# Optimization experiments

Measured on AMD Instinct MI355X. Metric: run time of the kernel, lower is better.

The kernel has to match this reference:

```python
import jax, jax.numpy as jnp
import numpy as np

H = 16  # num_attention_heads
LN_EPS = 1e-12


def setup_inputs() -> dict:
    key = jax.random.key(0)
    ks = jax.random.split(key, 13)
    S, B, D = 2048, 2, 1024
    std = 0.02
    return {
        "query_tensor": jax.random.normal(ks[0], (S, B, D), jnp.float32),
        "key_tensor": jax.random.normal(ks[1], (S, B, D), jnp.float32),
        "value_tensor": jax.random.normal(ks[2], (S, B, D), jnp.float32),
        "Wq": jax.random.normal(ks[3], (D, D), jnp.float32) * std,
        "bq": jnp.zeros((D,), jnp.float32),
        "Wk": jax.random.normal(ks[4], (D, D), jnp.float32) * std,
        "bk": jnp.zeros((D,), jnp.float32),
        "Wv": jax.random.normal(ks[5], (D, D), jnp.float32) * std,
        "bv": jnp.zeros((D,), jnp.float32),
        "Wo": jax.random.normal(ks[6], (D, D), jnp.float32) * std,
        "bo": jnp.zeros((D,), jnp.float32),
        "ln_w": jnp.ones((D,), jnp.float32),
        "ln_b": jnp.zeros((D,), jnp.float32),
    }


def _layernorm(x, w, b):
    u = jnp.mean(x, axis=-1, keepdims=True)
    s = jnp.mean(jnp.square(x - u), axis=-1, keepdims=True)
    return w * ((x - u) / jnp.sqrt(s + LN_EPS)) + b


def reference(query_tensor, key_tensor, value_tensor, Wq, bq, Wk, bk, Wv, bv, Wo, bo, ln_w, ln_b):
    S, B, D = query_tensor.shape
    dh = D // H
    # QKV projections (nn.Linear: x @ W.T + b)
    q = query_tensor @ Wq.T + bq          # (S, B, D)
    k = key_tensor @ Wk.T + bk            # (Sk, B, D)
    v = value_tensor @ Wv.T + bv          # (Sk, B, D)
    # (S, B, D) -> (B*H, S, dh)
    q = q.reshape(S, B * H, dh).transpose(1, 0, 2)
    k = k.reshape(-1, B * H, dh).transpose(1, 0, 2)
    v = v.reshape(-1, B * H, dh).transpose(1, 0, 2)
    # NOTE: original code has NO 1/sqrt(dh) scaling
    scores = jnp.einsum('nqd,nkd->nqk', q, k)            # (B*H, S, Sk)
    probs = jax.nn.softmax(scores, axis=-1)
    # dropout is identity in eval mode
    ctx = jnp.einsum('nqk,nkd->nqd', probs, v)           # (B*H, S, dh)
    ctx = ctx.transpose(1, 0, 2).reshape(S, B, D)
    # BertSelfOutput: dense + residual + LayerNorm (dropout identity)
    out = ctx @ Wo.T + bo
    return _layernorm(out + query_tensor, ln_w, ln_b)
```

## Files before the change

### kernel.cpp

```cpp
#include <hip/hip_runtime.h>

#define SEQ    2048
#define BATCH  2
#define DMODEL 1024
#define NHEAD  16
#define DH     64
#define MROWS  (SEQ*BATCH)
#define RS     (BATCH*DMODEL)
#define LN_EPS 1e-12f

typedef __attribute__((ext_vector_type(8))) short short8;
typedef __attribute__((ext_vector_type(4))) float floatx4;

#define AS_GLOBAL __attribute__((address_space(1)))
#define AS_LDS    __attribute__((address_space(3)))

__device__ __forceinline__ float bf2f(unsigned short s) {
    union { unsigned u; float f; } a; a.u = ((unsigned)s) << 16; return a.f;
}
__device__ __forceinline__ unsigned short f2bf(float x) {
    union { float f; unsigned u; } a; a.f = x;
    unsigned r = a.u + 0x7fffu + ((a.u >> 16) & 1u);
    return (unsigned short)(r >> 16);
}
__device__ __forceinline__ unsigned cvt_pk_bf16(float a, float b) {
    unsigned r;
    asm("v_cvt_pk_bf16_f32 %0, %1, %2" : "=v"(r) : "v"(a), "v"(b));
    return r;
}
__device__ __forceinline__ uint4 cvt8(const float* __restrict__ p) {
    float4 x0 = *(const float4*)(p);
    float4 x1 = *(const float4*)(p + 4);
    union { uint4 u; unsigned short s[8]; } r;
    r.s[0] = f2bf(x0.x); r.s[1] = f2bf(x0.y);
    r.s[2] = f2bf(x0.z); r.s[3] = f2bf(x0.w);
    r.s[4] = f2bf(x1.x); r.s[5] = f2bf(x1.y);
    r.s[6] = f2bf(x1.z); r.s[7] = f2bf(x1.w);
    return r.u;
}

__global__ void beacon_kernel(float* out, float val) {
    if (threadIdx.x == 0) out[0] = val;
}

__global__ __launch_bounds__(256)
void cvt_kernel(const float* __restrict__ s0, const float* __restrict__ s1,
                const float* __restrict__ s2, const float* __restrict__ s3,
                const float* __restrict__ s4, const float* __restrict__ s5,
                const float* __restrict__ s6,
                unsigned short* __restrict__ d0, unsigned short* __restrict__ d1,
                unsigned short* __restrict__ d2, unsigned short* __restrict__ d3,
                unsigned short* __restrict__ d4, unsigned short* __restrict__ d5,
                unsigned short* __restrict__ d6)
{
    const float* srcs[7] = {s0, s1, s2, s3, s4, s5, s6};
    unsigned short* dsts[7] = {d0, d1, d2, d3, d4, d5, d6};
    const int cnts[7] = {4194304, 4194304, 4194304, 1048576, 1048576, 1048576, 1048576};
    const int z = blockIdx.z;
    const float* src = srcs[z];
    unsigned short* dst = dsts[z];
    const int count = cnts[z];
    const int stride = gridDim.x * 256 * 8;
    for (int i = (blockIdx.x * 256 + threadIdx.x) * 8; i < count; i += stride)
        *(uint4*)&dst[i] = cvt8(&src[i]);
}

__global__ __launch_bounds__(256)
void vt_kernel(const unsigned short* __restrict__ Vb,
               unsigned short* __restrict__ VT)
{
    __shared__ __align__(16) short T[64*72];
    const int tid = threadIdx.x;
    const int s0 = blockIdx.x * 64;
    const int bh = blockIdx.y;
    const int b = bh >> 4, h = bh & 15;

    #pragma unroll
    for (int rep = 0; rep < 2; ++rep) {
        int c = tid + rep * 256;
        int s = c >> 3, cc = c & 7;
        *(uint4*)&T[s*72 + cc*8] =
            *(const uint4*)&Vb[((s0 + s) * BATCH + b) * DMODEL + h*64 + cc*8];
    }
    __syncthreads();
    #pragma unroll
    for (int rep = 0; rep < 2; ++rep) {
        int o = tid + rep * 256;
        int d = o >> 3, sc = o & 7;
        union { uint4 u; unsigned short e[8]; } pk;
        #pragma unroll
        for (int j = 0; j < 8; ++j)
            pk.e[j] = (unsigned short)T[(sc*8 + j)*72 + d];
        *(uint4*)&VT[bh*(DH*SEQ) + d*SEQ + s0 + sc*8] = pk.u;
    }
}

template<int OUTF32>
__device__ __forceinline__ void gemm_bf16_body(
    const unsigned short* __restrict__ A,
    const unsigned short* __restrict__ W,
    const float* __restrict__ bias,
    void* __restrict__ Cout)
{
    __shared__ __align__(16) short Alds[128*32];
    __shared__ __align__(16) short Blds[128*32];

    const int tid  = threadIdx.x;
    const int lane = tid & 63;
    const int wave = tid >> 6;
    const int lrow = lane & 15;
    const int lq   = lane >> 4;
    const int m0 = blockIdx.x * 128;
    const int n0 = blockIdx.y * 128;
    const int mw = (wave >> 1) * 64;
    const int nw = (wave & 1) * 64;
    const int K  = DMODEL;

    const int chunk0 = tid;
    const int chunk1 = tid + 256;
    const int row0 = chunk0 >> 2, col0 = (chunk0 & 3) << 3;
    const int row1 = chunk1 >> 2, col1 = (chunk1 & 3) << 3;
    const unsigned short* gA0 = &A[(m0 + row0) * K + col0];
    const unsigned short* gA1 = &A[(m0 + row1) * K + col1];
    const unsigned short* gB0 = &W[(n0 + row0) * K + col0];
    const unsigned short* gB1 = &W[(n0 + row1) * K + col1];
    AS_LDS unsigned int* lA0 = (AS_LDS unsigned int*)&Alds[(wave*64)*8];
    AS_LDS unsigned int* lA1 = (AS_LDS unsigned int*)&Alds[(256 + wave*64)*8];
    AS_LDS unsigned int* lB0 = (AS_LDS unsigned int*)&Blds[(wave*64)*8];
    AS_LDS unsigned int* lB1 = (AS_LDS unsigned int*)&Blds[(256 + wave*64)*8];

    floatx4 zero = {0.f, 0.f, 0.f, 0.f};
    floatx4 acc[4][4];
    #pragma unroll
    for (int i = 0; i < 4; ++i)
        #pragma unroll
        for (int j = 0; j < 4; ++j) acc[i][j] = zero;

    for (int k0 = 0; k0 < K; k0 += 32) {
        __builtin_amdgcn_global_load_lds((const AS_GLOBAL unsigned int*)(gA0 + k0), lA0, 16, 0, 0);
        __builtin_amdgcn_global_load_lds((const AS_GLOBAL unsigned int*)(gA1 + k0), lA1, 16, 0, 0);
        __builtin_amdgcn_global_load_lds((const AS_GLOBAL unsigned int*)(gB0 + k0), lB0, 16, 0, 0);
        __builtin_amdgcn_global_load_lds((const AS_GLOBAL unsigned int*)(gB1 + k0), lB1, 16, 0, 0);
        __syncthreads();
        short8 af[4], bfg[4];
        #pragma unroll
        for (int mi = 0; mi < 4; ++mi)
            af[mi] = *(const short8*)&Alds[(mw + mi*16 + lrow)*32 + lq*8];
        #pragma unroll
        for (int ni = 0; ni < 4; ++ni)
            bfg[ni] = *(const short8*)&Blds[(nw + ni*16 + lrow)*32 + lq*8];
        #pragma unroll
        for (int mi = 0; mi < 4; ++mi)
            #pragma unroll
            for (int ni = 0; ni < 4; ++ni)
                acc[mi][ni] = __builtin_amdgcn_mfma_f32_16x16x32_bf16(af[mi], bfg[ni], acc[mi][ni], 0, 0, 0);
        __syncthreads();
    }

    #pragma unroll
    for (int mi = 0; mi < 4; ++mi) {
        #pragma unroll
        for (int ni = 0; ni < 4; ++ni) {
            int n = n0 + nw + ni*16 + lrow;
            float bv_ = bias[n];
            #pragma unroll
            for (int r = 0; r < 4; ++r) {
                int m = m0 + mw + mi*16 + lq*4 + r;
                float v = acc[mi][ni][r] + bv_;
                if (OUTF32) ((float*)Cout)[m * DMODEL + n] = v;
                else ((unsigned short*)Cout)[m * DMODEL + n] = f2bf(v);
            }
        }
    }
}

__global__ __launch_bounds__(256)
void qkv_bf16(const unsigned short* __restrict__ qb, const unsigned short* __restrict__ kb,
              const unsigned short* __restrict__ vb,
              const unsigned short* __restrict__ Wqb, const float* __restrict__ bq,
              const unsigned short* __restrict__ Wkb, const float* __restrict__ bk,
              const unsigned short* __restrict__ Wvb, const float* __restrict__ bv,
              unsigned short* __restrict__ Qo, unsigned short* __restrict__ Ko,
              unsigned short* __restrict__ Vo)
{
    const unsigned short *A, *W; const float* B; unsigned short* C;
    if (blockIdx.z == 0)      { A = qb; W = Wqb; B = bq; C = Qo; }
    else if (blockIdx.z == 1) { A = kb; W = Wkb; B = bk; C = Ko; }
    else                      { A = vb; W = Wvb; B = bv; C = Vo; }
    gemm_bf16_body<0>(A, W, B, C);
}

__global__ __launch_bounds__(256)
void oproj_bf16(const unsigned short* __restrict__ Cx,
                const unsigned short* __restrict__ Wob, const float* __restrict__ bo,
                float* __restrict__ O32)
{
    gemm_bf16_body<1>(Cx, Wob, bo, O32);
}

__global__ __launch_bounds__(256)
void qkv_mfma(const float* __restrict__ q_in, const float* __restrict__ k_in,
              const float* __restrict__ v_in,
              const float* __restrict__ Wq, const float* __restrict__ bq,
              const float* __restrict__ Wk, const float* __restrict__ bk,
              const float* __restrict__ Wv, const float* __restrict__ bv,
              unsigned short* __restrict__ Qo, unsigned short* __restrict__ Ko,
              unsigned short* __restrict__ Vo)
{
    const float *A, *W, *B; unsigned short* C;
    if (blockIdx.z == 0)      { A = q_in; W = Wq; B = bq; C = Qo; }
    else if (blockIdx.z == 1) { A = k_in; W = Wk; B = bk; C = Ko; }
    else                      { A = v_in; W = Wv; B = bv; C = Vo; }

    __shared__ __align__(16) short Alds[128*32];
    __shared__ __align__(16) short Blds[128*32];
    const int tid  = threadIdx.x;
    const int lane = tid & 63;
    const int wave = tid >> 6;
    const int lrow = lane & 15;
    const int lq   = lane >> 4;
    const int m0 = blockIdx.x * 128;
    const int n0 = blockIdx.y * 128;
    const int mw = (wave >> 1) * 64;
    const int nw = (wave & 1) * 64;
    const int K  = DMODEL;

    floatx4 zero = {0.f, 0.f, 0.f, 0.f};
    floatx4 acc[4][4];
    #pragma unroll
    for (int i = 0; i < 4; ++i)
        #pragma unroll
        for (int j = 0; j < 4; ++j) acc[i][j] = zero;

    for (int k0 = 0; k0 < K; k0 += 32) {
        #pragma unroll
        for (int rep = 0; rep < 2; ++rep) {
            int chunk = tid + rep * 256;
            int row = chunk >> 2;
            int col = (chunk & 3) << 3;
            *(uint4*)&Alds[row*32 + col] = cvt8(&A[(m0 + row) * K + k0 + col]);
            *(uint4*)&Blds[row*32 + col] = cvt8(&W[(n0 + row) * K + k0 + col]);
        }
        __syncthreads();
        short8 af[4], bfg[4];
        #pragma unroll
        for (int mi = 0; mi < 4; ++mi)
            af[mi] = *(const short8*)&Alds[(mw + mi*16 + lrow)*32 + lq*8];
        #pragma unroll
        for (int ni = 0; ni < 4; ++ni)
            bfg[ni] = *(const short8*)&Blds[(nw + ni*16 + lrow)*32 + lq*8];
        #pragma unroll
        for (int mi = 0; mi < 4; ++mi)
            #pragma unroll
            for (int ni = 0; ni < 4; ++ni)
                acc[mi][ni] = __builtin_amdgcn_mfma_f32_16x16x32_bf16(af[mi], bfg[ni], acc[mi][ni], 0, 0, 0);
        __syncthreads();
    }

    #pragma unroll
    for (int mi = 0; mi < 4; ++mi) {
        #pragma unroll
        for (int ni = 0; ni < 4; ++ni) {
            int n = n0 + nw + ni*16 + lrow;
            float bv_ = B[n];
            #pragma unroll
            for (int r = 0; r < 4; ++r) {
                int m = m0 + mw + mi*16 + lq*4 + r;
                C[m * DMODEL + n] = f2bf(acc[mi][ni][r] + bv_);
            }
        }
    }
}

__global__ __launch_bounds__(256)
void oproj_mfma(const unsigned short* __restrict__ Cx,
                const float* __restrict__ Wo, const float* __restrict__ bo,
                float* __restrict__ O32)
{
    __shared__ __align__(16) short Alds[128*32];
    __shared__ __align__(16) short Blds[128*32];
    const int tid  = threadIdx.x;
    const int lane = tid & 63;
    const int wave = tid >> 6;
    const int lrow = lane & 15;
    const int lq   = lane >> 4;
    const int m0 = blockIdx.x * 128;
    const int n0 = blockIdx.y * 128;
    const int mw = (wave >> 1) * 64;
    const int nw = (wave & 1) * 64;
    const int K  = DMODEL;

    floatx4 zero = {0.f, 0.f, 0.f, 0.f};
    floatx4 acc[4][4];
    #pragma unroll
    for (int i = 0; i < 4; ++i)
        #pragma unroll
        for (int j = 0; j < 4; ++j) acc[i][j] = zero;

    for (int k0 = 0; k0 < K; k0 += 32) {
        #pragma unroll
        for (int rep = 0; rep < 2; ++rep) {
            int chunk = tid + rep * 256;
            int row = chunk >> 2;
            int col = (chunk & 3) << 3;
            *(uint4*)&Alds[row*32 + col] = *(const uint4*)&Cx[(m0 + row) * K + k0 + col];
            *(uint4*)&Blds[row*32 + col] = cvt8(&Wo[(n0 + row) * K + k0 + col]);
        }
        __syncthreads();
        short8 af[4], bfg[4];
        #pragma unroll
        for (int mi = 0; mi < 4; ++mi)
            af[mi] = *(const short8*)&Alds[(mw + mi*16 + lrow)*32 + lq*8];
        #pragma unroll
        for (int ni = 0; ni < 4; ++ni)
            bfg[ni] = *(const short8*)&Blds[(nw + ni*16 + lrow)*32 + lq*8];
        #pragma unroll
        for (int mi = 0; mi < 4; ++mi)
            #pragma unroll
            for (int ni = 0; ni < 4; ++ni)
                acc[mi][ni] = __builtin_amdgcn_mfma_f32_16x16x32_bf16(af[mi], bfg[ni], acc[mi][ni], 0, 0, 0);
        __syncthreads();
    }

    #pragma unroll
    for (int mi = 0; mi < 4; ++mi) {
        #pragma unroll
        for (int ni = 0; ni < 4; ++ni) {
            int n = n0 + nw + ni*16 + lrow;
            float bv_ = bo[n];
            #pragma unroll
            for (int r = 0; r < 4; ++r) {
                int m = m0 + mw + mi*16 + lq*4 + r;
                O32[m * DMODEL + n] = acc[mi][ni][r] + bv_;
            }
        }
    }
}

__global__ __launch_bounds__(256)
void attn_mfma4(const unsigned short* __restrict__ Q,
                const unsigned short* __restrict__ Kg,
                const unsigned short* __restrict__ VT,
                unsigned short* __restrict__ Ctx)
{
    __shared__ __align__(16) short SMEM[20480];

    const int tid  = threadIdx.x;
    const int lane = tid & 63;
    const int wave = tid >> 6;
    const int lrow = lane & 15;
    const int lq   = lane >> 4;

    const int q0 = blockIdx.x * 64;
    const int bh = blockIdx.y;
    const int off = (bh >> 4) * DMODEL + (bh & 15) * DH;
    const unsigned short* VTb = VT + bh * (DH * SEQ);
    short* const psw = &SMEM[16384 + wave * 1024];

    auto stageKV = [&](int kt, int b) {
        const int kbase = kt * 64;
        short* ksb = &SMEM[b * 8192];
        short* vtb = &SMEM[b * 8192 + 4096];
        #pragma unroll
        for (int rep = 0; rep < 2; ++rep) {
            int c = rep*256 + tid;
            int r = c >> 3, cc = c & 7;
            int sw = ((cc ^ (r & 7)) << 3);
            __builtin_amdgcn_global_load_lds(
                (const AS_GLOBAL unsigned int*)&Kg[(kbase + r) * RS + off + sw],
                (AS_LDS unsigned int*)&ksb[(rep*256 + wave*64) * 8], 16, 0, 0);
            __builtin_amdgcn_global_load_lds(
                (const AS_GLOBAL unsigned int*)&VTb[r * SEQ + kbase + sw],
                (AS_LDS unsigned int*)&vtb[(rep*256 + wave*64) * 8], 16, 0, 0);
        }
    };

    stageKV(0, 0);

    const int qrow = q0 + wave*16 + lrow;
    short8 qf[2];
    qf[0] = *(const short8*)&Q[qrow * RS + off + lq*8];
    qf[1] = *(const short8*)&Q[qrow * RS + off + 32 + lq*8];

    floatx4 zero = {0.f, 0.f, 0.f, 0.f};
    float m_i = -1e30f, l_i = 0.f;
    floatx4 oacc[4];
    #pragma unroll
    for (int ni = 0; ni < 4; ++ni) oacc[ni] = zero;

    __syncthreads();

    for (int kt = 0; kt < SEQ/64; ++kt) {
        const int cur = kt & 1;
        if (kt + 1 < SEQ/64) stageKV(kt + 1, cur ^ 1);
        const short* ksb = &SMEM[cur * 8192];
        const short* vtb = &SMEM[cur * 8192 + 4096];

        floatx4 sacc[4];
        #pragma unroll
        for (int ni = 0; ni < 4; ++ni) sacc[ni] = zero;
        __builtin_amdgcn_s_setprio(1);
        #pragma unroll
        for (int ni = 0; ni < 4; ++ni) {
            #pragma unroll
            for (int kk = 0; kk < 2; ++kk) {
                int key = ni*16 + lrow;
                int cc  = kk*4 + lq;
                short8 kf = *(const short8*)&ksb[key*64 + ((cc ^ (key & 7)) << 3)];
                sacc[ni] = __builtin_amdgcn_mfma_f32_16x16x32_bf16(kf, qf[kk], sacc[ni], 0, 0, 0);
            }
        }
        __builtin_amdgcn_s_setprio(0);

        float mx = sacc[0][0];
        #pragma unroll
        for (int ni = 0; ni < 4; ++ni)
            #pragma unroll
            for (int r = 0; r < 4; ++r) mx = fmaxf(mx, sacc[ni][r]);
        mx = fmaxf(mx, __shfl_xor(mx, 16));
        mx = fmaxf(mx, __shfl_xor(mx, 32));
        if (!__all(mx <= m_i + 8.f)) {
            float mnew = fmaxf(m_i, mx);
            float alpha = __expf(m_i - mnew);
            l_i *= alpha;
            #pragma unroll
            for (int ni = 0; ni < 4; ++ni)
                #pragma unroll
                for (int r = 0; r < 4; ++r) oacc[ni][r] *= alpha;
            m_i = mnew;
        }
        float p[4][4];
        float psum = 0.f;
        #pragma unroll
        for (int ni = 0; ni < 4; ++ni)
            #pragma unroll
            for (int r = 0; r < 4; ++r) {
                p[ni][r] = __expf(sacc[ni][r] - m_i);
                psum += p[ni][r];
            }
        psum += __shfl_xor(psum, 16);
        psum += __shfl_xor(psum, 32);
        l_i += psum;

        #pragma unroll
        for (int ni = 0; ni < 4; ++ni) {
            uint2 pk;
            pk.x = cvt_pk_bf16(p[ni][0], p[ni][1]);
            pk.y = cvt_pk_bf16(p[ni][2], p[ni][3]);
            int t  = ni*2 + (lq >> 1);
            int tp = t ^ (lrow & 7);
            *(uint2*)&psw[lrow*64 + tp*8 + (lq & 1)*4] = pk;
        }
        __builtin_amdgcn_wave_barrier();

        short8 pf[2];
        #pragma unroll
        for (int kk = 0; kk < 2; ++kk) {
            int t  = kk*4 + lq;
            int tp = t ^ (lrow & 7);
            pf[kk] = *(const short8*)&psw[lrow*64 + tp*8];
        }

        __builtin_amdgcn_s_setprio(1);
        #pragma unroll
        for (int ni = 0; ni < 4; ++ni) {
            #pragma unroll
            for (int kk = 0; kk < 2; ++kk) {
                int d  = ni*16 + lrow;
                int cc = kk*4 + lq;
                short8 vf = *(const short8*)&vtb[d*64 + ((cc ^ (d & 7)) << 3)];
                oacc[ni] = __builtin_amdgcn_mfma_f32_16x16x32_bf16(vf, pf[kk], oacc[ni], 0, 0, 0);
            }
        }
        __builtin_amdgcn_s_setprio(0);

        __syncthreads();
    }

    const float inv = 1.f / l_i;
    #pragma unroll
    for (int ni = 0; ni < 4; ++ni) {
        uint2 ok;
        ok.x = cvt_pk_bf16(oacc[ni][0] * inv, oacc[ni][1] * inv);
        ok.y = cvt_pk_bf16(oacc[ni][2] * inv, oacc[ni][3] * inv);
        *(uint2*)&Ctx[qrow * RS + off + ni*16 + lq*4] = ok;
    }
}

__global__ __launch_bounds__(256)
void attn_mfma2(const unsigned short* __restrict__ Q,
                const unsigned short* __restrict__ Kg,
                const unsigned short* __restrict__ V,
                unsigned short* __restrict__ Ctx)
{
    __shared__ __align__(16) short Qs[64*72];
    __shared__ __align__(16) short Ks[64*72];
    __shared__ __align__(16) short Vt[64*72];
    __shared__ __align__(16) short Ps[4][16*72];

    const int tid  = threadIdx.x;
    const int lane = tid & 63;
    const int wave = tid >> 6;
    const int lrow = lane & 15;
    const int lq   = lane >> 4;

    const int q0 = blockIdx.x * 64;
    const int bh = blockIdx.y;
    const int off = (bh >> 4) * DMODEL + (bh & 15) * DH;

    #pragma unroll
    for (int rep = 0; rep < 2; ++rep) {
        int chunk = tid + rep * 256;
        int r = chunk >> 3;
        int c = (chunk & 7) << 3;
        *(uint4*)&Qs[r*72 + c] = *(const uint4*)&Q[(q0 + r) * RS + off + c];
    }
    __syncthreads();

    short8 qf[2];
    #pragma unroll
    for (int ks = 0; ks < 2; ++ks)
        qf[ks] = *(const short8*)&Qs[(wave*16 + lrow)*72 + ks*32 + lq*8];

    floatx4 zero = {0.f, 0.f, 0.f, 0.f};
    float m_i = -1e30f, l_i = 0.f;
    floatx4 oacc[4];
    #pragma unroll
    for (int ni = 0; ni < 4; ++ni) oacc[ni] = zero;

    for (int kt = 0; kt < SEQ/64; ++kt) {
        __syncthreads();
        const int kbase = kt * 64;
        #pragma unroll
        for (int rep = 0; rep < 2; ++rep) {
            int chunk = tid + rep * 256;
            int r = chunk >> 3;
            int c = (chunk & 7) << 3;
            *(uint4*)&Ks[r*72 + c] = *(const uint4*)&Kg[(kbase + r) * RS + off + c];
            uint4 vv = *(const uint4*)&V[(kbase + r) * RS + off + c];
            union { uint4 u; short s[8]; } uv; uv.u = vv;
            int swz = (chunk & 7) << 3;
            #pragma unroll
            for (int j = 0; j < 8; ++j)
                Vt[(c + j)*72 + (r ^ swz)] = uv.s[j];
        }
        __syncthreads();

        floatx4 sacc[4];
        #pragma unroll
        for (int ni = 0; ni < 4; ++ni) sacc[ni] = zero;
        #pragma unroll
        for (int ni = 0; ni < 4; ++ni) {
            #pragma unroll
            for (int ks = 0; ks < 2; ++ks) {
                short8 kf = *(const short8*)&Ks[(ni*16 + lrow)*72 + ks*32 + lq*8];
                sacc[ni] = __builtin_amdgcn_mfma_f32_16x16x32_bf16(kf, qf[ks], sacc[ni], 0, 0, 0);
            }
        }

        float mx = sacc[0][0];
        #pragma unroll
        for (int ni = 0; ni < 4; ++ni)
            #pragma unroll
            for (int r = 0; r < 4; ++r) mx = fmaxf(mx, sacc[ni][r]);
        mx = fmaxf(mx, __shfl_xor(mx, 16));
        mx = fmaxf(mx, __shfl_xor(mx, 32));
        float mnew = fmaxf(m_i, mx);
        float alpha = __expf(m_i - mnew);
        float p[4][4];
        float psum = 0.f;
        #pragma unroll
        for (int ni = 0; ni < 4; ++ni)
            #pragma unroll
            for (int r = 0; r < 4; ++r) {
                p[ni][r] = __expf(sacc[ni][r] - mnew);
                psum += p[ni][r];
            }
        psum += __shfl_xor(psum, 16);
        psum += __shfl_xor(psum, 32);
        l_i = l_i * alpha + psum;
        m_i = mnew;
        #pragma unroll
        for (int ni = 0; ni < 4; ++ni)
            #pragma unroll
            for (int r = 0; r < 4; ++r) oacc[ni][r] *= alpha;

        #pragma unroll
        for (int ni = 0; ni < 4; ++ni) {
            uint2 pk;
            pk.x = (unsigned)f2bf(p[ni][0]) | ((unsigned)f2bf(p[ni][1]) << 16);
            pk.y = (unsigned)f2bf(p[ni][2]) | ((unsigned)f2bf(p[ni][3]) << 16);
            *(uint2*)&Ps[wave][lrow*72 + ni*16 + lq*4] = pk;
        }
        __builtin_amdgcn_wave_barrier();

        short8 pf[2];
        #pragma unroll
        for (int ks = 0; ks < 2; ++ks)
            pf[ks] = *(const short8*)&Ps[wave][lrow*72 + ks*32 + lq*8];
        #pragma unroll
        for (int ni = 0; ni < 4; ++ni) {
            #pragma unroll
            for (int ks = 0; ks < 2; ++ks) {
                int d  = ni*16 + lrow;
                int kk = ks*32 + lq*8;
                int swz = ((d >> 3) & 7) << 3;
                short8 vf = *(const short8*)&Vt[d*72 + (kk ^ swz)];
                oacc[ni] = __builtin_amdgcn_mfma_f32_16x16x32_bf16(vf, pf[ks], oacc[ni], 0, 0, 0);
            }
        }
    }

    const float inv = 1.f / l_i;
    const int q = q0 + wave*16 + lrow;
    #pragma unroll
    for (int ni = 0; ni < 4; ++ni) {
        uint2 ok;
        ok.x = (unsigned)f2bf(oacc[ni][0] * inv) | ((unsigned)f2bf(oacc[ni][1] * inv) << 16);
        ok.y = (unsigned)f2bf(oacc[ni][2] * inv) | ((unsigned)f2bf(oacc[ni][3] * inv) << 16);
        *(uint2*)&Ctx[q * RS + off + ni*16 + lq*4] = ok;
    }
}

__global__ __launch_bounds__(256)
void ln2_kernel(const float* __restrict__ O,
                const float* __restrict__ resid,
                const float* __restrict__ w,
                const float* __restrict__ bb,
                float* __restrict__ out)
{
    __shared__ float r1s[4];
    __shared__ float r2s[4];
    const int row = blockIdx.x;
    const int tid = threadIdx.x;
    const int c4 = tid * 4;

    float4 o4 = *(const float4*)&O[row * DMODEL + c4];
    float4 q4 = *(const float4*)&resid[row * DMODEL + c4];
    float x0 = o4.x + q4.x;
    float x1 = o4.y + q4.y;
    float x2 = o4.z + q4.z;
    float x3 = o4.w + q4.w;

    float s1 = x0 + x1 + x2 + x3;
    float s2 = x0*x0 + x1*x1 + x2*x2 + x3*x3;
    #pragma unroll
    for (int o = 32; o > 0; o >>= 1) {
        s1 += __shfl_xor(s1, o);
        s2 += __shfl_xor(s2, o);
    }
    if ((tid & 63) == 0) { r1s[tid >> 6] = s1; r2s[tid >> 6] = s2; }
    __syncthreads();
    float t1 = r1s[0] + r1s[1] + r1s[2] + r1s[3];
    float t2 = r2s[0] + r2s[1] + r2s[2] + r2s[3];

    const float mean = t1 * (1.f / DMODEL);
    float var = t2 * (1.f / DMODEL) - mean * mean;
    var = fmaxf(var, 0.f);
    const float rstd = rsqrtf(var + LN_EPS);

    float4 w4 = *(const float4*)&w[c4];
    float4 b4 = *(const float4*)&bb[c4];
    float4 y;
    y.x = w4.x * ((x0 - mean) * rstd) + b4.x;
    y.y = w4.y * ((x1 - mean) * rstd) + b4.y;
    y.z = w4.z * ((x2 - mean) * rstd) + b4.z;
    y.w = w4.w * ((x3 - mean) * rstd) + b4.w;
    *(float4*)&out[row * DMODEL + c4] = y;
}

extern "C" void kernel_launch(void* const* d_in, const int* in_sizes, int n_in,
                              void* d_out, int out_size, void* d_ws, size_t ws_size,
                              hipStream_t stream) {
    const float* q_in = (const float*)d_in[0];
    const float* k_in = (const float*)d_in[1];
    const float* v_in = (const float*)d_in[2];
    const float* Wq = (const float*)d_in[3];  const float* bq = (const float*)d_in[4];
    const float* Wk = (const float*)d_in[5];  const float* bk = (const float*)d_in[6];
    const float* Wv = (const float*)d_in[7];  const float* bv = (const float*)d_in[8];
    const float* Wo = (const float*)d_in[9];  const float* bo = (const float*)d_in[10];
    const float* lnw = (const float*)d_in[11]; const float* lnb = (const float*)d_in[12];

    char* wsb = (char*)d_ws;
    unsigned short* QCtx = (unsigned short*)d_out;
    float*          outF = (float*)d_out;
    dim3 blk(256);

    if (ws_size >= (48u << 20)) {
        unsigned short* qb  = (unsigned short*)(wsb);
        unsigned short* kb  = (unsigned short*)(wsb + (8u  << 20));
        unsigned short* vb  = (unsigned short*)(wsb + (16u << 20));
        unsigned short* Wqb = (unsigned short*)(wsb + (24u << 20));
        unsigned short* Wkb = (unsigned short*)(wsb + (26u << 20));
        unsigned short* Wvb = (unsigned short*)(wsb + (28u << 20));
        unsigned short* Wob = (unsigned short*)(wsb + (30u << 20));
        unsigned short* Kb  = (unsigned short*)(wsb + (32u << 20));
        unsigned short* Vb  = (unsigned short*)(wsb + (40u << 20));
        unsigned short* VT  = (unsigned short*)(wsb);
        float*          O32 = (float*)(wsb);

        cvt_kernel<<<dim3(512, 1, 7), blk, 0, stream>>>(
            q_in, k_in, v_in, Wq, Wk, Wv, Wo,
            qb, kb, vb, Wqb, Wkb, Wvb, Wob);
        qkv_bf16<<<dim3(MROWS/128, DMODEL/128, 3), blk, 0, stream>>>(
            qb, kb, vb, Wqb, bq, Wkb, bk, Wvb, bv, QCtx, Kb, Vb);
        vt_kernel<<<dim3(SEQ/64, BATCH*NHEAD), blk, 0, stream>>>(Vb, VT);
        attn_mfma4<<<dim3(SEQ/64, BATCH*NHEAD), blk, 0, stream>>>(QCtx, Kb, VT, QCtx);
        oproj_bf16<<<dim3(MROWS/128, DMODEL/128), blk, 0, stream>>>(QCtx, Wob, bo, O32);
        ln2_kernel<<<dim3(MROWS), blk, 0, stream>>>(O32, q_in, lnw, lnb, outF);
    } else if (ws_size >= (16u << 20)) {
        unsigned short* Kb  = (unsigned short*)(wsb);
        unsigned short* Vb  = (unsigned short*)(wsb + (8u << 20));
        float*          O32 = (float*)(wsb);
        qkv_mfma<<<dim3(MROWS/128, DMODEL/128, 3), blk, 0, stream>>>(
            q_in, k_in, v_in, Wq, bq, Wk, bk, Wv, bv, QCtx, Kb, Vb);
        attn_mfma2<<<dim3(SEQ/64, BATCH*NHEAD), blk, 0, stream>>>(QCtx, Kb, Vb, QCtx);
        oproj_mfma<<<dim3(MROWS/128, DMODEL/128), blk, 0, stream>>>(QCtx, Wo, bo, O32);
        ln2_kernel<<<dim3(MROWS), blk, 0, stream>>>(O32, q_in, lnw, lnb, outF);
    } else {
        beacon_kernel<<<1, 64, 0, stream>>>((float*)d_out, 300.0f);
    }
}
```

Before: 256.8 us.

## Fold log2e into Wq, use exp2 softmax with max-initialized accumulators, double-buffer GEMM LDS

Scales Wq and bq by log2(e) during conversion so attention scores come out in base-2 units, and the softmax uses the hardware exp2 directly. The running max is subtracted by seeding the MFMA accumulators with -m_i, and the max reduction uses v_max3. The GEMM body moves to double-buffered LDS with a prefetch of the next K-slice. This trims VALU work in the softmax and overlaps global loads with MFMA in the projections. The trade-offs are extra LDS and the extra rounding from scaling Wq before the bf16 conversion.

```diff
diff --git a/kernel.cpp b/kernel.cpp
--- a/kernel.cpp
+++ b/kernel.cpp
@@ -8,6 +8,7 @@
 #define MROWS  (SEQ*BATCH)
 #define RS     (BATCH*DMODEL)
 #define LN_EPS 1e-12f
+#define LOG2E  1.4426950408889634f
 
 typedef __attribute__((ext_vector_type(8))) short short8;
 typedef __attribute__((ext_vector_type(4))) float floatx4;
@@ -27,6 +28,18 @@
     unsigned r;
     asm("v_cvt_pk_bf16_f32 %0, %1, %2" : "=v"(r) : "v"(a), "v"(b));
     return r;
+}
+__device__ __forceinline__ float max3f(float a, float b, float c) {
+    float r;
+    asm("v_max3_f32 %0, %1, %2, %3" : "=v"(r) : "v"(a), "v"(b), "v"(c));
+    return r;
+}
+__device__ __forceinline__ float fast_exp2(float x) {
+#if __has_builtin(__builtin_amdgcn_exp2f)
+    return __builtin_amdgcn_exp2f(x);
+#else
+    return exp2f(x);
+#endif
 }
 __device__ __forceinline__ uint4 cvt8(const float* __restrict__ p) {
     float4 x0 = *(const float4*)(p);
@@ -38,6 +51,16 @@
     r.s[6] = f2bf(x1.z); r.s[7] = f2bf(x1.w);
     return r.u;
 }
+__device__ __forceinline__ uint4 cvt8s(const float* __restrict__ p, float sc) {
+    float4 x0 = *(const float4*)(p);
+    float4 x1 = *(const float4*)(p + 4);
+    union { uint4 u; unsigned short s[8]; } r;
+    r.s[0] = f2bf(x0.x*sc); r.s[1] = f2bf(x0.y*sc);
+    r.s[2] = f2bf(x0.z*sc); r.s[3] = f2bf(x0.w*sc);
+    r.s[4] = f2bf(x1.x*sc); r.s[5] = f2bf(x1.y*sc);
+    r.s[6] = f2bf(x1.z*sc); r.s[7] = f2bf(x1.w*sc);
+    return r.u;
+}
 
 __global__ void beacon_kernel(float* out, float val) {
     if (threadIdx.x == 0) out[0] = val;
@@ -56,13 +79,15 @@
     const float* srcs[7] = {s0, s1, s2, s3, s4, s5, s6};
     unsigned short* dsts[7] = {d0, d1, d2, d3, d4, d5, d6};
     const int cnts[7] = {4194304, 4194304, 4194304, 1048576, 1048576, 1048576, 1048576};
+    const float scl[7] = {1.f, 1.f, 1.f, LOG2E, 1.f, 1.f, 1.f};
     const int z = blockIdx.z;
     const float* src = srcs[z];
     unsigned short* dst = dsts[z];
     const int count = cnts[z];
+    const float sc = scl[z];
     const int stride = gridDim.x * 256 * 8;
     for (int i = (blockIdx.x * 256 + threadIdx.x) * 8; i < count; i += stride)
-        *(uint4*)&dst[i] = cvt8(&src[i]);
+        *(uint4*)&dst[i] = cvt8s(&src[i], sc);
 }
 
 __global__ __launch_bounds__(256)
@@ -99,11 +124,11 @@
 __device__ __forceinline__ void gemm_bf16_body(
     const unsigned short* __restrict__ A,
     const unsigned short* __restrict__ W,
-    const float* __restrict__ bias,
+    const float* __restrict__ bias, float bscale,
     void* __restrict__ Cout)
 {
-    __shared__ __align__(16) short Alds[128*32];
-    __shared__ __align__(16) short Blds[128*32];
+    __shared__ __align__(16) short Alds[2][128*32];
+    __shared__ __align__(16) short Blds[2][128*32];
 
     const int tid  = threadIdx.x;
     const int lane = tid & 63;
@@ -124,10 +149,17 @@
     const unsigned short* gA1 = &A[(m0 + row1) * K + col1];
     const unsigned short* gB0 = &W[(n0 + row0) * K + col0];
     const unsigned short* gB1 = &W[(n0 + row1) * K + col1];
-    AS_LDS unsigned int* lA0 = (AS_LDS unsigned int*)&Alds[(wave*64)*8];
-    AS_LDS unsigned int* lA1 = (AS_LDS unsigned int*)&Alds[(256 + wave*64)*8];
-    AS_LDS unsigned int* lB0 = (AS_LDS unsigned int*)&Blds[(wave*64)*8];
-    AS_LDS unsigned int* lB1 = (AS_LDS unsigned int*)&Blds[(256 + wave*64)*8];
+
+    auto stage = [&](int k0, int b) {
+        __builtin_amdgcn_global_load_lds((const AS_GLOBAL unsigned int*)(gA0 + k0),
+            (AS_LDS unsigned int*)&Alds[b][(wave*64)*8], 16, 0, 0);
+        __builtin_amdgcn_global_load_lds((const AS_GLOBAL unsigned int*)(gA1 + k0),
+            (AS_LDS unsigned int*)&Alds[b][(256 + wave*64)*8], 16, 0, 0);
+        __builtin_amdgcn_global_load_lds((const AS_GLOBAL unsigned int*)(gB0 + k0),
+            (AS_LDS unsigned int*)&Blds[b][(wave*64)*8], 16, 0, 0);
+        __builtin_amdgcn_global_load_lds((const AS_GLOBAL unsigned int*)(gB1 + k0),
+            (AS_LDS unsigned int*)&Blds[b][(256 + wave*64)*8], 16, 0, 0);
+    };
 
     floatx4 zero = {0.f, 0.f, 0.f, 0.f};
     floatx4 acc[4][4];
@@ -136,19 +168,19 @@
         #pragma unroll
         for (int j = 0; j < 4; ++j) acc[i][j] = zero;
 
+    stage(0, 0);
+    __syncthreads();
+
     for (int k0 = 0; k0 < K; k0 += 32) {
-        __builtin_amdgcn_global_load_lds((const AS_GLOBAL unsigned int*)(gA0 + k0), lA0, 16, 0, 0);
-        __builtin_amdgcn_global_load_lds((const AS_GLOBAL unsigned int*)(gA1 + k0), lA1, 16, 0, 0);
-        __builtin_amdgcn_global_load_lds((const AS_GLOBAL unsigned int*)(gB0 + k0), lB0, 16, 0, 0);
-        __builtin_amdgcn_global_load_lds((const AS_GLOBAL unsigned int*)(gB1 + k0), lB1, 16, 0, 0);
-        __syncthreads();
+        const int cur = (k0 >> 5) & 1;
+        if (k0 + 32 < K) stage(k0 + 32, cur ^ 1);
         short8 af[4], bfg[4];
         #pragma unroll
         for (int mi = 0; mi < 4; ++mi)
-            af[mi] = *(const short8*)&Alds[(mw + mi*16 + lrow)*32 + lq*8];
+            af[mi] = *(const short8*)&Alds[cur][(mw + mi*16 + lrow)*32 + lq*8];
         #pragma unroll
         for (int ni = 0; ni < 4; ++ni)
-            bfg[ni] = *(const short8*)&Blds[(nw + ni*16 + lrow)*32 + lq*8];
+            bfg[ni] = *(const short8*)&Blds[cur][(nw + ni*16 + lrow)*32 + lq*8];
         #pragma unroll
         for (int mi = 0; mi < 4; ++mi)
             #pragma unroll
@@ -162,7 +194,7 @@
         #pragma unroll
         for (int ni = 0; ni < 4; ++ni) {
             int n = n0 + nw + ni*16 + lrow;
-            float bv_ = bias[n];
+            float bv_ = bias[n] * bscale;
             #pragma unroll
             for (int r = 0; r < 4; ++r) {
                 int m = m0 + mw + mi*16 + lq*4 + r;
@@ -183,11 +215,11 @@
               unsigned short* __restrict__ Qo, unsigned short* __restrict__ Ko,
               unsigned short* __restrict__ Vo)
 {
-    const unsigned short *A, *W; const float* B; unsigned short* C;
-    if (blockIdx.z == 0)      { A = qb; W = Wqb; B = bq; C = Qo; }
-    else if (blockIdx.z == 1) { A = kb; W = Wkb; B = bk; C = Ko; }
-    else                      { A = vb; W = Wvb; B = bv; C = Vo; }
-    gemm_bf16_body<0>(A, W, B, C);
+    const unsigned short *A, *W; const float* B; unsigned short* C; float bs;
+    if (blockIdx.z == 0)      { A = qb; W = Wqb; B = bq; C = Qo; bs = LOG2E; }
+    else if (blockIdx.z == 1) { A = kb; W = Wkb; B = bk; C = Ko; bs = 1.f; }
+    else                      { A = vb; W = Wvb; B = bv; C = Vo; bs = 1.f; }
+    gemm_bf16_body<0>(A, W, B, bs, C);
 }
 
 __global__ __launch_bounds__(256)
@@ -195,7 +227,7 @@
                 const unsigned short* __restrict__ Wob, const float* __restrict__ bo,
                 float* __restrict__ O32)
 {
-    gemm_bf16_body<1>(Cx, Wob, bo, O32);
+    gemm_bf16_body<1>(Cx, Wob, bo, 1.f, O32);
 }
 
 __global__ __launch_bounds__(256)
@@ -338,7 +370,7 @@
 }
 
 __global__ __launch_bounds__(256)
-void attn_mfma4(const unsigned short* __restrict__ Q,
+void attn_mfma5(const unsigned short* __restrict__ Q,
                 const unsigned short* __restrict__ Kg,
                 const unsigned short* __restrict__ VT,
                 unsigned short* __restrict__ Ctx)
@@ -383,7 +415,7 @@
     qf[1] = *(const short8*)&Q[qrow * RS + off + 32 + lq*8];
 
     floatx4 zero = {0.f, 0.f, 0.f, 0.f};
-    float m_i = -1e30f, l_i = 0.f;
+    float m_i = 0.f, l_i = 0.f;
     floatx4 oacc[4];
     #pragma unroll
     for (int ni = 0; ni < 4; ++ni) oacc[ni] = zero;
@@ -397,8 +429,10 @@
         const short* vtb = &SMEM[cur * 8192 + 4096];
 
         floatx4 sacc[4];
-        #pragma unroll
-        for (int ni = 0; ni < 4; ++ni) sacc[ni] = zero;
+        const float negm = -m_i;
+        floatx4 minit = {negm, negm, negm, negm};
+        #pragma unroll
+        for (int ni = 0; ni < 4; ++ni) sacc[ni] = minit;
         __builtin_amdgcn_s_setprio(1);
         #pragma unroll
         for (int ni = 0; ni < 4; ++ni) {
@@ -412,32 +446,45 @@
         }
         __builtin_amdgcn_s_setprio(0);
 
-        float mx = sacc[0][0];
-        #pragma unroll
-        for (int ni = 0; ni < 4; ++ni)
-            #pragma unroll
-            for (int r = 0; r < 4; ++r) mx = fmaxf(mx, sacc[ni][r]);
+        float a0 = max3f(sacc[0][0], sacc[0][1], sacc[0][2]);
+        float a1 = max3f(sacc[0][3], sacc[1][0], sacc[1][1]);
+        float a2 = max3f(sacc[1][2], sacc[1][3], sacc[2][0]);
+        float a3 = max3f(sacc[2][1], sacc[2][2], sacc[2][3]);
+        float a4 = max3f(sacc[3][0], sacc[3][1], sacc[3][2]);
+        float b0 = max3f(a0, a1, a2);
+        float b1 = max3f(a3, a4, sacc[3][3]);
+        float mx = fmaxf(b0, b1);
         mx = fmaxf(mx, __shfl_xor(mx, 16));
         mx = fmaxf(mx, __shfl_xor(mx, 32));
-        if (!__all(mx <= m_i + 8.f)) {
-            float mnew = fmaxf(m_i, mx);
-            float alpha = __expf(m_i - mnew);
+
+        float p[4][4];
+        if (__all(mx <= 8.f)) {
+            #pragma unroll
+            for (int ni = 0; ni < 4; ++ni)
+                #pragma unroll
+                for (int r = 0; r < 4; ++r)
+                    p[ni][r] = fast_exp2(sacc[ni][r]);
+        } else {
+            float shift = fmaxf(mx, 0.f);
+            float alpha = fast_exp2(-shift);
             l_i *= alpha;
             #pragma unroll
             for (int ni = 0; ni < 4; ++ni)
                 #pragma unroll
                 for (int r = 0; r < 4; ++r) oacc[ni][r] *= alpha;
-            m_i = mnew;
-        }
-        float p[4][4];
-        float psum = 0.f;
-        #pragma unroll
-        for (int ni = 0; ni < 4; ++ni)
-            #pragma unroll
-            for (int r = 0; r < 4; ++r) {
-                p[ni][r] = __expf(sacc[ni][r] - m_i);
-                psum += p[ni][r];
-            }
+            m_i += shift;
+            #pragma unroll
+            for (int ni = 0; ni < 4; ++ni)
+                #pragma unroll
+                for (int r = 0; r < 4; ++r)
+                    p[ni][r] = fast_exp2(sacc[ni][r] - shift);
+        }
+
+        float s00 = (p[0][0] + p[0][1]) + (p[0][2] + p[0][3]);
+        float s01 = (p[1][0] + p[1][1]) + (p[1][2] + p[1][3]);
+        float s10 = (p[2][0] + p[2][1]) + (p[2][2] + p[2][3]);
+        float s11 = (p[3][0] + p[3][1]) + (p[3][2] + p[3][3]);
+        float psum = (s00 + s01) + (s10 + s11);
         psum += __shfl_xor(psum, 16);
         psum += __shfl_xor(psum, 32);
         l_i += psum;
@@ -705,7 +752,7 @@
         qkv_bf16<<<dim3(MROWS/128, DMODEL/128, 3), blk, 0, stream>>>(
             qb, kb, vb, Wqb, bq, Wkb, bk, Wvb, bv, QCtx, Kb, Vb);
         vt_kernel<<<dim3(SEQ/64, BATCH*NHEAD), blk, 0, stream>>>(Vb, VT);
-        attn_mfma4<<<dim3(SEQ/64, BATCH*NHEAD), blk, 0, stream>>>(QCtx, Kb, VT, QCtx);
+        attn_mfma5<<<dim3(SEQ/64, BATCH*NHEAD), blk, 0, stream>>>(QCtx, Kb, VT, QCtx);
         oproj_bf16<<<dim3(MROWS/128, DMODEL/128), blk, 0, stream>>>(QCtx, Wob, bo, O32);
         ln2_kernel<<<dim3(MROWS), blk, 0, stream>>>(O32, q_in, lnw, lnb, outF);
     } else if (ws_size >= (16u << 20)) {
```

New measurement: 259.1 us. No clear change (+0.9%).
